# Kernel optimization log

Hardware: AMD Instinct MI355X
Metric: run time of the kernel (lower is better)

Reference implementation:

```python
import jax, jax.numpy as jnp
import numpy as np

B, MAXN = 4096, 10
NVT, MAXPOS = 26, 9          # max_pos + 1
HS, NZ = 301, 56
EMB, FEAT = 16, 8
VS = HS + MAXPOS             # hidden || pos one-hot fed to gate/mapper
XDIM = NVT + MAXPOS          # GRU input dim
DF = 3 * MAXPOS              # r/c/gm per position
GS = HS + FEAT


def _gru(x, h, W_ih, W_hh, b_ih, b_hh):
    # torch.nn.GRUCell semantics (gate order r, z, n)
    gi = x @ W_ih.T + b_ih
    gh = h @ W_hh.T + b_hh
    ir, iz, inn = jnp.split(gi, 3, axis=-1)
    hr, hz, hn = jnp.split(gh, 3, axis=-1)
    rg = jax.nn.sigmoid(ir + hr)
    zg = jax.nn.sigmoid(iz + hz)
    ng = jnp.tanh(inn + rg * hn)
    return (1.0 - zg) * ng + zg * h


def setup_inputs() -> dict:
    key = jax.random.key(0)
    ks = jax.random.split(key, 32)
    def gl(k, shape, fan_in):
        return (jax.random.normal(k, shape, jnp.float32) / np.sqrt(fan_in)).astype(jnp.float32)
    inp = {
        'node_type': jax.random.randint(ks[0], (B, MAXN), 0, NVT),
        'pos':       jax.random.randint(ks[1], (B, MAXN), 0, MAXPOS),
        'adj':       jax.random.randint(ks[2], (B, MAXN, MAXN), 0, 2).astype(jnp.int32),
        'vcount':    jax.random.randint(ks[3], (B,), 0, MAXN),
        'r':  jax.random.uniform(ks[4], (B, MAXN), jnp.float32),
        'c':  jax.random.uniform(ks[5], (B, MAXN), jnp.float32),
        'gm': jax.random.uniform(ks[6], (B, MAXN), jnp.float32),
        # grue_forward (GRUCell)
        'W_ih': gl(ks[7], (3 * HS, XDIM), XDIM),
        'W_hh': gl(ks[8], (3 * HS, HS), HS),
        'b_ih': jnp.zeros((3 * HS,), jnp.float32),
        'b_hh': jnp.zeros((3 * HS,), jnp.float32),
        # gate_forward (Linear + sigmoid) and mapper_forward (Linear, no bias)
        'Wg': gl(ks[9], (HS, VS), VS),
        'bg': jnp.zeros((HS,), jnp.float32),
        'Wm': gl(ks[10], (HS, VS), VS),
        # df_enc: Linear(27,16) ReLU Linear(16,8)
        'W1': gl(ks[11], (EMB, DF), DF),
        'b1': jnp.zeros((EMB,), jnp.float32),
        'W2': gl(ks[12], (FEAT, EMB), EMB),
        'b2': jnp.zeros((FEAT,), jnp.float32),
        # fc1 / fc2 heads
        'Wmu': gl(ks[13], (NZ, GS), GS),
        'bmu': jnp.zeros((NZ,), jnp.float32),
        'Wlv': gl(ks[14], (NZ, GS), GS),
        'blv': jnp.zeros((NZ,), jnp.float32),
    }
    return inp


def reference(node_type, pos, adj, vcount, r, c, gm,
              W_ih, W_hh, b_ih, b_hh, Wg, bg, Wm,
              W1, b1, W2, b2, Wmu, bmu, Wlv, blv):
    n = jnp.clip(vcount, 1, MAXN).astype(jnp.int32)          # graphs have >=1 vertex
    node_ids = jnp.arange(MAXN)
    valid = node_ids[None, :] < n[:, None]                   # [B, MAXN] vertex exists
    tri = node_ids[:, None] < node_ids[None, :]              # u < v (topological DAG)
    A = (adj.astype(jnp.float32) * tri
         * valid[:, :, None] * valid[:, None, :])            # [B, u, v] pred mask

    t_oh = jax.nn.one_hot(node_type, NVT, dtype=jnp.float32)
    p_oh = jax.nn.one_hot(pos, MAXPOS, dtype=jnp.float32)
    X = jnp.concatenate([t_oh, p_oh], axis=-1)               # [B, MAXN, XDIM]

    H = jnp.zeros((B, MAXN, HS), jnp.float32)
    for v in range(MAXN):
        if v == 0:
            Hin = jnp.zeros((B, HS), jnp.float32)            # H0 in encode()
        else:
            # gated predecessor aggregation: sum_u gate(h_u||pos_u)*mapper(h_u||pos_u)
            Hcat = jnp.concatenate([H[:, :v], p_oh[:, :v]], axis=-1)   # [B, v, VS]
            gated = (jax.nn.sigmoid(jnp.einsum('bud,hd->buh', Hcat, Wg) + bg)
                     * jnp.einsum('bud,hd->buh', Hcat, Wm))            # [B, v, HS]
            Hin = jnp.einsum('bu,buh->bh', A[:, :v, v], gated)
        Hv = _gru(X[:, v], Hin, W_ih, W_hh, b_ih, b_hh)
        H = H.at[:, v].set(jnp.where(valid[:, v][:, None], Hv, H[:, v]))

    # graph state: H_forward of last existing vertex
    Hg = H[jnp.arange(B), n - 1]                             # [B, HS]

    # df feature: per-position (r, c, gm), later vertices overwrite earlier ones
    df = jnp.zeros((B, DF), jnp.float32)
    bi = jnp.arange(B)
    for v in range(MAXN):
        m = valid[:, v][:, None]
        for k, val in enumerate((r[:, v], c[:, v], gm[:, v])):
            upd = df.at[bi, pos[:, v] * 3 + k].set(val)
            df = jnp.where(m, upd, df)

    Hd = jax.nn.relu(df @ W1.T + b1) @ W2.T + b2             # df_enc
    Hfull = jnp.concatenate([Hg, Hd], axis=-1)               # [B, GS]
    mu = Hfull @ Wmu.T + bmu
    logvar = Hfull @ Wlv.T + blv
    return mu, logvar
```

## Files before the change

kernel.cpp:

```cpp
#include <hip/hip_runtime.h>
#include <hip/hip_bf16.h>


#define HS 301
#define NVT 26
#define MAXPOS 9
#define MAXN 10
#define BSZ 4096
#define VS 310
#define GS 309
#define NZ 56

#define KT1 11
#define KT2 10
#define NJT 19
#define NB1 (NJT*KT1*3*512)
#define NB2 (NJT*KT2*2*512)

typedef _Float16 f16x8 __attribute__((ext_vector_type(8)));
typedef float f32x4 __attribute__((ext_vector_type(4)));

constexpr int NTH  = 1024;
constexpr int BT   = 16;
constexpr int NBLK = 256;

__device__ __forceinline__ int fragOff(int g, int k) {
  return ((k >> 5) << 10) + ((((k & 31) >> 3) << 4) + g) * 16 + ((k & 7) << 1);
}
__device__ __forceinline__ float sigm(float x) { return 1.0f / (1.0f + __expf(-x)); }
__device__ __forceinline__ float tanh_fast(float x) {
  float e = __expf(2.0f * x);
  return 1.0f - 2.0f / (e + 1.0f);
}
#define BC(x) __builtin_bit_cast(f16x8, (x))

__global__ void ckt_sort(const int* __restrict__ vcount, int* __restrict__ order) {
  __shared__ int cnt[12], off[12];
  int tid = threadIdx.x;
  if (tid < 12) cnt[tid] = 0;
  __syncthreads();
  for (int g = tid; g < BSZ; g += 1024) {
    int n = vcount[g]; n = n < 1 ? 1 : (n > MAXN ? MAXN : n);
    atomicAdd(&cnt[n], 1);
  }
  __syncthreads();
  if (tid == 0) {
    int s = 0;
    for (int i = 1; i <= MAXN; ++i) { off[i] = s; s += cnt[i]; }
  }
  __syncthreads();
  for (int g = tid; g < BSZ; g += 1024) {
    int n = vcount[g]; n = n < 1 ? 1 : (n > MAXN ? MAXN : n);
    int p = atomicAdd(&off[n], 1);
    order[p] = g;
  }
}

__global__ void ckt_prep(const float* __restrict__ Wih, const float* __restrict__ Whh,
                         const float* __restrict__ b_ih, const float* __restrict__ b_hh,
                         const float* __restrict__ Wg,  const float* __restrict__ bg,
                         const float* __restrict__ Wm,
                         const float* __restrict__ Wmu, const float* __restrict__ Wlv,
                         unsigned short* __restrict__ B1, unsigned short* __restrict__ B2,
                         float* __restrict__ WnX, float* __restrict__ bn,
                         float* __restrict__ WmuT, float* __restrict__ WlvT)
{
  int i0 = blockIdx.x * blockDim.x + threadIdx.x;
  int str = gridDim.x * blockDim.x;
  for (int i = i0; i < NB1; i += str) {
    int ii = i & 7, lane = (i >> 3) & 63;
    int r = i >> 9;
    int g3 = r % 3; r /= 3;
    int kt = r % KT1; int jt = r / KT1;
    int j = jt * 16 + (lane & 15);
    int k = kt * 32 + ((lane >> 4) << 3) + ii;
    float val = 0.f;
    if (j < HS) {
      int row = g3 * HS + j;
      if (k < HS) val = Whh[row * HS + k];
      else if (k == 336) val = (g3 < 2) ? (b_ih[row] + b_hh[row]) : b_hh[row];
      else if (g3 < 2) {
        if (k < 327)      val = Wih[row * 35 + (k - 301)];
        else if (k < 336) val = Wih[row * 35 + 26 + (k - 327)];
      }
    }
    B1[i] = __builtin_bit_cast(unsigned short, (_Float16)val);
  }
  for (int i = i0; i < NB2; i += str) {
    int ii = i & 7, lane = (i >> 3) & 63;
    int r = i >> 9;
    int gm = r % 2; r /= 2;
    int kt = r % KT2; int jt = r / KT2;
    int j = jt * 16 + (lane & 15);
    int k = kt * 32 + ((lane >> 4) << 3) + ii;
    float val = 0.f;
    if (j < HS) {
      const float* W = gm ? Wm : Wg;
      if (k < HS)       val = W[j * VS + k];
      else if (k < 310) val = W[j * VS + HS + (k - 301)];
      else if (k == 310) val = gm ? 0.f : bg[j];
    }
    B2[i] = __builtin_bit_cast(unsigned short, (_Float16)val);
  }
  for (int i = i0; i < 35 * 320; i += str) {
    int x = i / 320, j = i % 320;
    WnX[i] = (j < HS) ? Wih[(2 * HS + j) * 35 + x] : 0.f;
  }
  for (int i = i0; i < 320; i += str) bn[i] = (i < HS) ? b_ih[2 * HS + i] : 0.f;
  for (int i = i0; i < GS * NZ; i += str) {
    int k = i / NZ, o = i % NZ;
    WmuT[i] = Wmu[o * GS + k];
    WlvT[i] = Wlv[o * GS + k];
  }
}

__global__ __launch_bounds__(NTH) void ckt_main(
    const int* __restrict__ node_type, const int* __restrict__ pos,
    const int* __restrict__ adj, const int* __restrict__ vcount,
    const float* __restrict__ rin, const float* __restrict__ cin,
    const float* __restrict__ gmin,
    const float* __restrict__ W1, const float* __restrict__ b1,
    const float* __restrict__ W2, const float* __restrict__ b2,
    const float* __restrict__ bmu, const float* __restrict__ blv,
    const uint4* __restrict__ B1, const uint4* __restrict__ B2,
    const float* __restrict__ WnX, const float* __restrict__ bnG,
    const float* __restrict__ WmuT, const float* __restrict__ WlvT,
    const int* __restrict__ order,
    float* __restrict__ out)
{
  __shared__ __align__(16) _Float16 sGhist[9 * 16 * 304];
  __shared__ __align__(16) char sAf1[KT1 * 1024];
  __shared__ __align__(16) char sAf2[KT2 * 1024];
  __shared__ __align__(16) _Float16 sHg[16 * 304];
  __shared__ float sBn[320];
  __shared__ int s_gi[16];
  __shared__ int s_t[160], s_p[160], s_n[16];
  __shared__ unsigned s_am[160];
  __shared__ int s_nmax;
  __shared__ float s_df[16][28];
  __shared__ float s_hd[16][16];
  __shared__ float s_hd2[16][8];

  const int tid  = threadIdx.x;
  const int b0   = blockIdx.x * BT;
  const int w    = tid >> 6;
  const int lane = tid & 63;

  if (tid < 16) s_gi[tid] = order[b0 + tid];
  __syncthreads();
  if (tid < 16) {
    int n = vcount[s_gi[tid]];
    s_n[tid] = n < 1 ? 1 : (n > MAXN ? MAXN : n);
    sHg[tid * 304 + 301] = (_Float16)0.f;
    sHg[tid * 304 + 302] = (_Float16)0.f;
    sHg[tid * 304 + 303] = (_Float16)0.f;
  }
  if (tid < 160) {
    int g = tid / 10, vv = tid % 10;
    s_t[tid] = node_type[s_gi[g] * MAXN + vv];
    s_p[tid] = pos[s_gi[g] * MAXN + vv];
  }
  if (tid < 320) sBn[tid] = bnG[tid];
  __syncthreads();
  if (tid < 160) {
    int g = tid / 10, vv = tid % 10;
    unsigned m = 0;
    if (vv < s_n[g]) {
      for (int u = 0; u < vv; ++u)
        if (adj[s_gi[g] * 100 + u * 10 + vv]) m |= (1u << u);
    }
    s_am[tid] = m;
  }
  if (tid == 0) {
    int mx = 1;
    for (int g = 0; g < 16; ++g) mx = max(mx, s_n[g]);
    s_nmax = mx;
  }
  __syncthreads();
  const int nmax = s_nmax;

  const int lq4 = (lane >> 4) << 2;
  const int jc  = lane & 15;

  for (int v = 0; v < nmax; ++v) {
    if (tid < KT1 * 64) {
      int c = tid;
      int kt = c >> 6, ln = c & 63, g = ln & 15;
      int k0 = (kt << 5) + ((ln >> 4) << 3);
      unsigned am = s_am[g * 10 + v];
      f16x8 pk;
      if (k0 + 8 <= HS) {
        float a0 = 0.f, a1 = 0.f, a2 = 0.f, a3 = 0.f;
        float a4 = 0.f, a5 = 0.f, a6 = 0.f, a7 = 0.f;
        for (int u = 0; u < v; ++u) {
          float mf = (float)((am >> u) & 1u);
          f16x8 hh = *(const f16x8*)(sGhist + (u * 16 + g) * 304 + k0);
          a0 += mf * (float)hh[0]; a1 += mf * (float)hh[1];
          a2 += mf * (float)hh[2]; a3 += mf * (float)hh[3];
          a4 += mf * (float)hh[4]; a5 += mf * (float)hh[5];
          a6 += mf * (float)hh[6]; a7 += mf * (float)hh[7];
        }
        pk[0] = (_Float16)a0; pk[1] = (_Float16)a1;
        pk[2] = (_Float16)a2; pk[3] = (_Float16)a3;
        pk[4] = (_Float16)a4; pk[5] = (_Float16)a5;
        pk[6] = (_Float16)a6; pk[7] = (_Float16)a7;
      } else {
        int t = s_t[g * 10 + v], p = s_p[g * 10 + v];
        #pragma unroll
        for (int e = 0; e < 8; ++e) {
          int k = k0 + e;
          float x = 0.f;
          if (k < HS) {
            for (int u = 0; u < v; ++u) {
              float mf = (float)((am >> u) & 1u);
              x += mf * (float)sGhist[(u * 16 + g) * 304 + k];
            }
          } else if (k < 327) x = (k - 301 == t) ? 1.f : 0.f;
          else if (k < 336)   x = (k - 327 == p) ? 1.f : 0.f;
          else if (k == 336)  x = 1.f;
          pk[e] = (_Float16)x;
        }
      }
      *(f16x8*)(sAf1 + c * 16) = pk;
    } else if (tid - KT1 * 64 < 16 * 19) {
      int i = tid - KT1 * 64;
      int g = i / 19, kk = 301 + i % 19;
      float val = (kk < 310) ? ((kk - 301 == s_p[g * 10 + v]) ? 1.f : 0.f)
                             : ((kk == 310) ? 1.f : 0.f);
      *(_Float16*)(sAf2 + fragOff(g, kk)) = (_Float16)val;
    }
    __syncthreads();

#define LB1(P0, P1, P2, KT) \
      P0 = BC(Bp[((KT) * 3 + 0) * 64]); \
      P1 = BC(Bp[((KT) * 3 + 1) * 64]); \
      P2 = BC(Bp[((KT) * 3 + 2) * 64]);
#define ST1(P0, P1, P2, KT, KTN) { \
      f16x8 av = *(const f16x8*)(sAf1 + (KT) * 1024 + lane * 16); \
      f16x8 c0 = P0, c1 = P1, c2 = P2; \
      LB1(P0, P1, P2, KTN) \
      a0 = __builtin_amdgcn_mfma_f32_16x16x32_f16(av, c0, a0, 0, 0, 0); \
      a1 = __builtin_amdgcn_mfma_f32_16x16x32_f16(av, c1, a1, 0, 0, 0); \
      a2 = __builtin_amdgcn_mfma_f32_16x16x32_f16(av, c2, a2, 0, 0, 0); }
#define ST1E(P0, P1, P2, KT) { \
      f16x8 av = *(const f16x8*)(sAf1 + (KT) * 1024 + lane * 16); \
      a0 = __builtin_amdgcn_mfma_f32_16x16x32_f16(av, P0, a0, 0, 0, 0); \
      a1 = __builtin_amdgcn_mfma_f32_16x16x32_f16(av, P1, a1, 0, 0, 0); \
      a2 = __builtin_amdgcn_mfma_f32_16x16x32_f16(av, P2, a2, 0, 0, 0); }
    for (int jj = w; jj < NJT; jj += 16) {
      const uint4* Bp = B1 + (size_t)jj * (KT1 * 3 * 64) + lane;
      f16x8 p00, p01, p02, p10, p11, p12, p20, p21, p22, p30, p31, p32;
      LB1(p00, p01, p02, 0) LB1(p10, p11, p12, 1)
      LB1(p20, p21, p22, 2) LB1(p30, p31, p32, 3)
      f32x4 a0 = {0.f, 0.f, 0.f, 0.f}, a1 = a0, a2 = a0;
      ST1(p00, p01, p02, 0, 4) ST1(p10, p11, p12, 1, 5)
      ST1(p20, p21, p22, 2, 6) ST1(p30, p31, p32, 3, 7)
      ST1(p00, p01, p02, 4, 8) ST1(p10, p11, p12, 5, 9)
      ST1(p20, p21, p22, 6, 10)
      ST1E(p30, p31, p32, 7) ST1E(p00, p01, p02, 8)
      ST1E(p10, p11, p12, 9) ST1E(p20, p21, p22, 10)
      int j = jj * 16 + jc;
      bool jv = j < HS;
      #pragma unroll
      for (int q = 0; q < 4; ++q) {
        int g = lq4 + q;
        float inn = 0.f;
        if (jv) {
          int t = s_t[g * 10 + v], p = s_p[g * 10 + v];
          inn = sBn[j] + WnX[t * 320 + j] + WnX[(26 + p) * 320 + j];
        }
        float rg = sigm(a0[q]);
        float zg = sigm(a1[q]);
        float ng = tanh_fast(inn + rg * a2[q]);
        float hinv = jv ? (float)*(const _Float16*)(sAf1 + fragOff(g, j)) : 0.f;
        float hv = (1.f - zg) * ng + zg * hinv;
        float hval = (v < s_n[g]) ? hv : 0.f;
        if (jv) {
          *(_Float16*)(sAf2 + fragOff(g, j)) = (_Float16)hval;
          if (v == s_n[g] - 1) sHg[g * 304 + j] = (_Float16)hv;
        }
      }
    }
#undef ST1
#undef ST1E
#undef LB1
    __syncthreads();

    if (v < nmax - 1) {
#define LB2(P0, P1, KT) \
        P0 = BC(Bp[((KT) * 2 + 0) * 64]); \
        P1 = BC(Bp[((KT) * 2 + 1) * 64]);
#define ST2(P0, P1, KT, KTN) { \
        f16x8 av = *(const f16x8*)(sAf2 + (KT) * 1024 + lane * 16); \
        f16x8 d0 = P0, d1 = P1; \
        LB2(P0, P1, KTN) \
        c0 = __builtin_amdgcn_mfma_f32_16x16x32_f16(av, d0, c0, 0, 0, 0); \
        c1 = __builtin_amdgcn_mfma_f32_16x16x32_f16(av, d1, c1, 0, 0, 0); }
#define ST2E(P0, P1, KT) { \
        f16x8 av = *(const f16x8*)(sAf2 + (KT) * 1024 + lane * 16); \
        c0 = __builtin_amdgcn_mfma_f32_16x16x32_f16(av, P0, c0, 0, 0, 0); \
        c1 = __builtin_amdgcn_mfma_f32_16x16x32_f16(av, P1, c1, 0, 0, 0); }
      for (int jj = w; jj < NJT; jj += 16) {
        const uint4* Bp = B2 + (size_t)jj * (KT2 * 2 * 64) + lane;
        f16x8 q00, q01, q10, q11, q20, q21, q30, q31;
        LB2(q00, q01, 0) LB2(q10, q11, 1) LB2(q20, q21, 2) LB2(q30, q31, 3)
        f32x4 c0 = {0.f, 0.f, 0.f, 0.f}, c1 = c0;
        ST2(q00, q01, 0, 4) ST2(q10, q11, 1, 5) ST2(q20, q21, 2, 6)
        ST2(q30, q31, 3, 7) ST2(q00, q01, 4, 8) ST2(q10, q11, 5, 9)
        ST2E(q20, q21, 6) ST2E(q30, q31, 7) ST2E(q00, q01, 8) ST2E(q10, q11, 9)
        int j = jj * 16 + jc;
        if (j < HS) {
          #pragma unroll
          for (int q = 0; q < 4; ++q) {
            int g = lq4 + q;
            float gg = sigm(c0[q]);
            sGhist[(v * 16 + g) * 304 + j] = (_Float16)(gg * c1[q]);
          }
        }
      }
#undef ST2
#undef ST2E
#undef LB2
    }
    __syncthreads();
  }

  if (tid < 16) {
    int g = tid;
    #pragma unroll
    for (int i2 = 0; i2 < 27; ++i2) s_df[g][i2] = 0.f;
    int n = s_n[g];
    int gi = s_gi[g];
    for (int vv = 0; vv < n; ++vv) {
      int p = s_p[g * 10 + vv];
      int base = gi * MAXN + vv;
      s_df[g][3 * p]     = rin[base];
      s_df[g][3 * p + 1] = cin[base];
      s_df[g][3 * p + 2] = gmin[base];
    }
  }
  __syncthreads();

  if (tid < 256) {
    int bb = tid >> 4, o = tid & 15;
    float a = b1[o];
    #pragma unroll
    for (int k = 0; k < 27; ++k) a = fmaf(W1[o * 27 + k], s_df[bb][k], a);
    s_hd[bb][o] = fmaxf(a, 0.f);
  }
  __syncthreads();
  if (tid < 128) {
    int bb = tid >> 3, o = tid & 7;
    float a = b2[o];
    #pragma unroll
    for (int k = 0; k < 16; ++k) a = fmaf(W2[o * 16 + k], s_hd[bb][k], a);
    s_hd2[bb][o] = a;
  }
  __syncthreads();

  if (tid < 2 * NZ) {
    bool ismu = tid < NZ;
    int oo = ismu ? tid : tid - NZ;
    const float* WT = ismu ? WmuT : WlvT;
    float acc[16];
    #pragma unroll
    for (int g = 0; g < 16; ++g) acc[g] = 0.f;
    for (int k0 = 0; k0 < 304; k0 += 8) {
      float wv[8];
      #pragma unroll
      for (int e = 0; e < 8; ++e) {
        int k = k0 + e;
        wv[e] = (k < HS) ? WT[k * NZ + oo] : 0.f;
      }
      #pragma unroll
      for (int g = 0; g < 16; ++g) {
        f16x8 hh = *(const f16x8*)(sHg + g * 304 + k0);
        #pragma unroll
        for (int e = 0; e < 8; ++e) acc[g] += wv[e] * (float)hh[e];
      }
    }
    #pragma unroll
    for (int g = 0; g < 16; ++g) {
      float a = acc[g];
      #pragma unroll
      for (int kk = 0; kk < 8; ++kk) a += WT[(HS + kk) * NZ + oo] * s_hd2[g][kk];
      a += ismu ? bmu[oo] : blv[oo];
      out[(ismu ? 0 : BSZ * NZ) + s_gi[g] * NZ + oo] = a;
    }
  }
}

extern "C" void kernel_launch(void* const* d_in, const int* in_sizes, int n_in,
                              void* d_out, int out_size, void* d_ws, size_t ws_size,
                              hipStream_t stream) {
  const int*   node_type = (const int*)d_in[0];
  const int*   pos       = (const int*)d_in[1];
  const int*   adj       = (const int*)d_in[2];
  const int*   vcount    = (const int*)d_in[3];
  const float* rin       = (const float*)d_in[4];
  const float* cin       = (const float*)d_in[5];
  const float* gmin      = (const float*)d_in[6];
  const float* Wih       = (const float*)d_in[7];
  const float* Whh       = (const float*)d_in[8];
  const float* b_ih      = (const float*)d_in[9];
  const float* b_hh      = (const float*)d_in[10];
  const float* Wg        = (const float*)d_in[11];
  const float* bg        = (const float*)d_in[12];
  const float* Wm        = (const float*)d_in[13];
  const float* W1        = (const float*)d_in[14];
  const float* b1        = (const float*)d_in[15];
  const float* W2        = (const float*)d_in[16];
  const float* b2        = (const float*)d_in[17];
  const float* Wmu       = (const float*)d_in[18];
  const float* bmu       = (const float*)d_in[19];
  const float* Wlv       = (const float*)d_in[20];
  const float* blv       = (const float*)d_in[21];

  char* wsb = (char*)d_ws;
  unsigned short* B1 = (unsigned short*)wsb;
  unsigned short* B2 = (unsigned short*)(wsb + 642048);
  float* WnX  = (float*)(wsb + 1031168);
  float* bn   = (float*)(wsb + 1075968);
  float* WmuT = (float*)(wsb + 1077248);
  float* WlvT = (float*)(wsb + 1146464);
  int*   order = (int*)(wsb + 1215680);

  ckt_prep<<<512, 256, 0, stream>>>(Wih, Whh, b_ih, b_hh, Wg, bg, Wm, Wmu, Wlv,
                                    B1, B2, WnX, bn, WmuT, WlvT);
  ckt_sort<<<1, 1024, 0, stream>>>(vcount, order);

  ckt_main<<<NBLK, NTH, 0, stream>>>(node_type, pos, adj, vcount, rin, cin, gmin,
      W1, b1, W2, b2, bmu, blv,
      (const uint4*)B1, (const uint4*)B2, WnX, bn, WmuT, WlvT, order, (float*)d_out);
}
```

Measured before the change: 162.2 us.

## Prefetch MFMA weight fragments across barriers and use LDS-only barrier waits

Issues the global loads for the first weight k-tiles of each wave's GRU and gate GEMMs before the preceding barrier, so their latency overlaps the A-fragment build and the GRU epilogue. The strided jj loops are split into an always-run first tile and a conditional second tile for waves 0-2. __syncthreads is replaced by an lgkmcnt-only wait plus s_barrier, so in-flight global loads are not drained at barriers. A waves_per_eu(4) attribute is added. Together these raise register pressure and lean on the hand-written waitcnt being correct.

```diff
diff --git a/kernel.cpp b/kernel.cpp
--- a/kernel.cpp
+++ b/kernel.cpp
@@ -33,6 +33,8 @@
   return 1.0f - 2.0f / (e + 1.0f);
 }
 #define BC(x) __builtin_bit_cast(f16x8, (x))
+#define BAR() { asm volatile("s_waitcnt lgkmcnt(0)" ::: "memory"); \
+                __builtin_amdgcn_s_barrier(); }
 
 __global__ void ckt_sort(const int* __restrict__ vcount, int* __restrict__ order) {
   __shared__ int cnt[12], off[12];
@@ -114,7 +116,9 @@
   }
 }
 
-__global__ __launch_bounds__(NTH) void ckt_main(
+__global__ __launch_bounds__(NTH)
+__attribute__((amdgpu_waves_per_eu(4)))
+void ckt_main(
     const int* __restrict__ node_type, const int* __restrict__ pos,
     const int* __restrict__ adj, const int* __restrict__ vcount,
     const float* __restrict__ rin, const float* __restrict__ cin,
@@ -181,8 +185,14 @@
 
   const int lq4 = (lane >> 4) << 2;
   const int jc  = lane & 15;
+  const uint4* BpW = B1 + (size_t)w * (KT1 * 3 * 64) + lane;
+  const uint4* BqW = B2 + (size_t)w * (KT2 * 2 * 64) + lane;
 
   for (int v = 0; v < nmax; ++v) {
+    f16x8 f00 = BC(BpW[0]),   f01 = BC(BpW[64]),  f02 = BC(BpW[128]);
+    f16x8 f10 = BC(BpW[192]), f11 = BC(BpW[256]), f12 = BC(BpW[320]);
+    f16x8 g00, g01, g10, g11;
+
     if (tid < KT1 * 64) {
       int c = tid;
       int kt = c >> 6, ln = c & 63, g = ln & 15;
@@ -229,7 +239,7 @@
                              : ((kk == 310) ? 1.f : 0.f);
       *(_Float16*)(sAf2 + fragOff(g, kk)) = (_Float16)val;
     }
-    __syncthreads();
+    BAR();
 
 #define LB1(P0, P1, P2, KT) \
       P0 = BC(Bp[((KT) * 3 + 0) * 64]); \
@@ -247,8 +257,44 @@
       a0 = __builtin_amdgcn_mfma_f32_16x16x32_f16(av, P0, a0, 0, 0, 0); \
       a1 = __builtin_amdgcn_mfma_f32_16x16x32_f16(av, P1, a1, 0, 0, 0); \
       a2 = __builtin_amdgcn_mfma_f32_16x16x32_f16(av, P2, a2, 0, 0, 0); }
-    for (int jj = w; jj < NJT; jj += 16) {
-      const uint4* Bp = B1 + (size_t)jj * (KT1 * 3 * 64) + lane;
+#define GRU_EPI(JT) { \
+      int j = (JT) * 16 + jc; \
+      bool jv = j < HS; \
+      _Pragma("unroll") \
+      for (int q = 0; q < 4; ++q) { \
+        int g = lq4 + q; \
+        float inn = 0.f; \
+        if (jv) { \
+          int t = s_t[g * 10 + v], p = s_p[g * 10 + v]; \
+          inn = sBn[j] + WnX[t * 320 + j] + WnX[(26 + p) * 320 + j]; \
+        } \
+        float rg = sigm(a0[q]); \
+        float zg = sigm(a1[q]); \
+        float ng = tanh_fast(inn + rg * a2[q]); \
+        float hinv = jv ? (float)*(const _Float16*)(sAf1 + fragOff(g, j)) : 0.f; \
+        float hv = (1.f - zg) * ng + zg * hinv; \
+        float hval = (v < s_n[g]) ? hv : 0.f; \
+        if (jv) { \
+          *(_Float16*)(sAf2 + fragOff(g, j)) = (_Float16)hval; \
+          if (v == s_n[g] - 1) sHg[g * 304 + j] = (_Float16)hv; \
+        } \
+      } }
+    {
+      const uint4* Bp = BpW;
+      f16x8 p20, p21, p22, p30, p31, p32;
+      LB1(p20, p21, p22, 2) LB1(p30, p31, p32, 3)
+      f32x4 a0 = {0.f, 0.f, 0.f, 0.f}, a1 = a0, a2 = a0;
+      ST1(f00, f01, f02, 0, 4) ST1(f10, f11, f12, 1, 5)
+      ST1(p20, p21, p22, 2, 6) ST1(p30, p31, p32, 3, 7)
+      ST1(f00, f01, f02, 4, 8) ST1(f10, f11, f12, 5, 9)
+      ST1(p20, p21, p22, 6, 10)
+      ST1E(p30, p31, p32, 7) ST1E(f00, f01, f02, 8)
+      ST1E(f10, f11, f12, 9) ST1E(p20, p21, p22, 10)
+      GRU_EPI(w)
+    }
+    if (w < 3) {
+      const int jt2 = w + 16;
+      const uint4* Bp = B1 + (size_t)jt2 * (KT1 * 3 * 64) + lane;
       f16x8 p00, p01, p02, p10, p11, p12, p20, p21, p22, p30, p31, p32;
       LB1(p00, p01, p02, 0) LB1(p10, p11, p12, 1)
       LB1(p20, p21, p22, 2) LB1(p30, p31, p32, 3)
@@ -259,32 +305,14 @@
       ST1(p20, p21, p22, 6, 10)
       ST1E(p30, p31, p32, 7) ST1E(p00, p01, p02, 8)
       ST1E(p10, p11, p12, 9) ST1E(p20, p21, p22, 10)
-      int j = jj * 16 + jc;
-      bool jv = j < HS;
-      #pragma unroll
-      for (int q = 0; q < 4; ++q) {
-        int g = lq4 + q;
-        float inn = 0.f;
-        if (jv) {
-          int t = s_t[g * 10 + v], p = s_p[g * 10 + v];
-          inn = sBn[j] + WnX[t * 320 + j] + WnX[(26 + p) * 320 + j];
-        }
-        float rg = sigm(a0[q]);
-        float zg = sigm(a1[q]);
-        float ng = tanh_fast(inn + rg * a2[q]);
-        float hinv = jv ? (float)*(const _Float16*)(sAf1 + fragOff(g, j)) : 0.f;
-        float hv = (1.f - zg) * ng + zg * hinv;
-        float hval = (v < s_n[g]) ? hv : 0.f;
-        if (jv) {
-          *(_Float16*)(sAf2 + fragOff(g, j)) = (_Float16)hval;
-          if (v == s_n[g] - 1) sHg[g * 304 + j] = (_Float16)hv;
-        }
-      }
+      GRU_EPI(jt2)
     }
 #undef ST1
 #undef ST1E
 #undef LB1
-    __syncthreads();
+    g00 = BC(BqW[0]);   g01 = BC(BqW[64]);
+    g10 = BC(BqW[128]); g11 = BC(BqW[192]);
+    BAR();
 
     if (v < nmax - 1) {
 #define LB2(P0, P1, KT) \
@@ -300,29 +328,42 @@
         f16x8 av = *(const f16x8*)(sAf2 + (KT) * 1024 + lane * 16); \
         c0 = __builtin_amdgcn_mfma_f32_16x16x32_f16(av, P0, c0, 0, 0, 0); \
         c1 = __builtin_amdgcn_mfma_f32_16x16x32_f16(av, P1, c1, 0, 0, 0); }
-      for (int jj = w; jj < NJT; jj += 16) {
-        const uint4* Bp = B2 + (size_t)jj * (KT2 * 2 * 64) + lane;
+#define GATE_EPI(JT) { \
+        int j = (JT) * 16 + jc; \
+        if (j < HS) { \
+          _Pragma("unroll") \
+          for (int q = 0; q < 4; ++q) { \
+            int g = lq4 + q; \
+            float gg = sigm(c0[q]); \
+            sGhist[(v * 16 + g) * 304 + j] = (_Float16)(gg * c1[q]); \
+          } \
+        } }
+      {
+        const uint4* Bp = BqW;
+        f16x8 q20, q21, q30, q31;
+        LB2(q20, q21, 2) LB2(q30, q31, 3)
+        f32x4 c0 = {0.f, 0.f, 0.f, 0.f}, c1 = c0;
+        ST2(g00, g01, 0, 4) ST2(g10, g11, 1, 5) ST2(q20, q21, 2, 6)
+        ST2(q30, q31, 3, 7) ST2(g00, g01, 4, 8) ST2(g10, g11, 5, 9)
+        ST2E(q20, q21, 6) ST2E(q30, q31, 7) ST2E(g00, g01, 8) ST2E(g10, g11, 9)
+        GATE_EPI(w)
+      }
+      if (w < 3) {
+        const int jt2 = w + 16;
+        const uint4* Bp = B2 + (size_t)jt2 * (KT2 * 2 * 64) + lane;
         f16x8 q00, q01, q10, q11, q20, q21, q30, q31;
         LB2(q00, q01, 0) LB2(q10, q11, 1) LB2(q20, q21, 2) LB2(q30, q31, 3)
         f32x4 c0 = {0.f, 0.f, 0.f, 0.f}, c1 = c0;
         ST2(q00, q01, 0, 4) ST2(q10, q11, 1, 5) ST2(q20, q21, 2, 6)
         ST2(q30, q31, 3, 7) ST2(q00, q01, 4, 8) ST2(q10, q11, 5, 9)
         ST2E(q20, q21, 6) ST2E(q30, q31, 7) ST2E(q00, q01, 8) ST2E(q10, q11, 9)
-        int j = jj * 16 + jc;
-        if (j < HS) {
-          #pragma unroll
-          for (int q = 0; q < 4; ++q) {
-            int g = lq4 + q;
-            float gg = sigm(c0[q]);
-            sGhist[(v * 16 + g) * 304 + j] = (_Float16)(gg * c1[q]);
-          }
-        }
+        GATE_EPI(jt2)
       }
 #undef ST2
 #undef ST2E
 #undef LB2
     }
-    __syncthreads();
+    BAR();
   }
 
   if (tid < 16) {
```

Measured after the change: 452.7 us. +179.1%, slower.

## Shrink block to four waves with deeper B prefetch and lighter barriers

Applied to the files above, without the earlier changes.

Cuts the main kernel from 1024 to 256 threads per block and requests a single block per CU via launch bounds. Each wave now loops over up to five 16-column j-tiles instead of at most two. The weight-fragment prefetch for both MFMA GEMMs becomes a six- or five-stage register pipeline. __syncthreads is replaced by an explicit lgkmcnt wait plus s_barrier. The aim is cheaper barriers and more registers for deeper prefetch, at the cost of fewer waves to hide latency and a longer serial chain per wave in each recurrence step.

```diff
diff --git a/kernel.cpp b/kernel.cpp
--- a/kernel.cpp
+++ b/kernel.cpp
@@ -20,7 +20,7 @@
 typedef _Float16 f16x8 __attribute__((ext_vector_type(8)));
 typedef float f32x4 __attribute__((ext_vector_type(4)));
 
-constexpr int NTH  = 1024;
+constexpr int NTH  = 256;
 constexpr int BT   = 16;
 constexpr int NBLK = 256;
 
@@ -33,6 +33,8 @@
   return 1.0f - 2.0f / (e + 1.0f);
 }
 #define BC(x) __builtin_bit_cast(f16x8, (x))
+#define BAR() { asm volatile("s_waitcnt lgkmcnt(0)" ::: "memory"); \
+                __builtin_amdgcn_s_barrier(); }
 
 __global__ void ckt_sort(const int* __restrict__ vcount, int* __restrict__ order) {
   __shared__ int cnt[12], off[12];
@@ -114,7 +116,7 @@
   }
 }
 
-__global__ __launch_bounds__(NTH) void ckt_main(
+__global__ __launch_bounds__(NTH, 1) void ckt_main(
     const int* __restrict__ node_type, const int* __restrict__ pos,
     const int* __restrict__ adj, const int* __restrict__ vcount,
     const float* __restrict__ rin, const float* __restrict__ cin,
@@ -160,7 +162,7 @@
     s_t[tid] = node_type[s_gi[g] * MAXN + vv];
     s_p[tid] = pos[s_gi[g] * MAXN + vv];
   }
-  if (tid < 320) sBn[tid] = bnG[tid];
+  for (int k = tid; k < 320; k += NTH) sBn[k] = bnG[k];
   __syncthreads();
   if (tid < 160) {
     int g = tid / 10, vv = tid % 10;
@@ -183,8 +185,7 @@
   const int jc  = lane & 15;
 
   for (int v = 0; v < nmax; ++v) {
-    if (tid < KT1 * 64) {
-      int c = tid;
+    for (int c = tid; c < KT1 * 64; c += NTH) {
       int kt = c >> 6, ln = c & 63, g = ln & 15;
       int k0 = (kt << 5) + ((ln >> 4) << 3);
       unsigned am = s_am[g * 10 + v];
@@ -222,43 +223,41 @@
         }
       }
       *(f16x8*)(sAf1 + c * 16) = pk;
-    } else if (tid - KT1 * 64 < 16 * 19) {
-      int i = tid - KT1 * 64;
+    }
+    for (int i = tid; i < 16 * 19; i += NTH) {
       int g = i / 19, kk = 301 + i % 19;
       float val = (kk < 310) ? ((kk - 301 == s_p[g * 10 + v]) ? 1.f : 0.f)
                              : ((kk == 310) ? 1.f : 0.f);
       *(_Float16*)(sAf2 + fragOff(g, kk)) = (_Float16)val;
     }
-    __syncthreads();
-
-#define LB1(P0, P1, P2, KT) \
-      P0 = BC(Bp[((KT) * 3 + 0) * 64]); \
-      P1 = BC(Bp[((KT) * 3 + 1) * 64]); \
-      P2 = BC(Bp[((KT) * 3 + 2) * 64]);
-#define ST1(P0, P1, P2, KT, KTN) { \
+    BAR();
+
+#define LD1(S0, S1, S2, KT) \
+      S0 = BC(Bp[((KT) * 3 + 0) * 64]); \
+      S1 = BC(Bp[((KT) * 3 + 1) * 64]); \
+      S2 = BC(Bp[((KT) * 3 + 2) * 64]);
+#define MF1(S0, S1, S2, KT) { \
       f16x8 av = *(const f16x8*)(sAf1 + (KT) * 1024 + lane * 16); \
-      f16x8 c0 = P0, c1 = P1, c2 = P2; \
-      LB1(P0, P1, P2, KTN) \
-      a0 = __builtin_amdgcn_mfma_f32_16x16x32_f16(av, c0, a0, 0, 0, 0); \
-      a1 = __builtin_amdgcn_mfma_f32_16x16x32_f16(av, c1, a1, 0, 0, 0); \
-      a2 = __builtin_amdgcn_mfma_f32_16x16x32_f16(av, c2, a2, 0, 0, 0); }
-#define ST1E(P0, P1, P2, KT) { \
-      f16x8 av = *(const f16x8*)(sAf1 + (KT) * 1024 + lane * 16); \
-      a0 = __builtin_amdgcn_mfma_f32_16x16x32_f16(av, P0, a0, 0, 0, 0); \
-      a1 = __builtin_amdgcn_mfma_f32_16x16x32_f16(av, P1, a1, 0, 0, 0); \
-      a2 = __builtin_amdgcn_mfma_f32_16x16x32_f16(av, P2, a2, 0, 0, 0); }
-    for (int jj = w; jj < NJT; jj += 16) {
+      a0 = __builtin_amdgcn_mfma_f32_16x16x32_f16(av, S0, a0, 0, 0, 0); \
+      a1 = __builtin_amdgcn_mfma_f32_16x16x32_f16(av, S1, a1, 0, 0, 0); \
+      a2 = __builtin_amdgcn_mfma_f32_16x16x32_f16(av, S2, a2, 0, 0, 0); }
+    for (int r = 0; r < 5; ++r) {
+      int jj = w + 4 * r;
+      if (jj >= NJT) break;
       const uint4* Bp = B1 + (size_t)jj * (KT1 * 3 * 64) + lane;
-      f16x8 p00, p01, p02, p10, p11, p12, p20, p21, p22, p30, p31, p32;
-      LB1(p00, p01, p02, 0) LB1(p10, p11, p12, 1)
-      LB1(p20, p21, p22, 2) LB1(p30, p31, p32, 3)
+      f16x8 s00,s01,s02, s10,s11,s12, s20,s21,s22,
+            s30,s31,s32, s40,s41,s42, s50,s51,s52;
+      LD1(s00,s01,s02, 0) LD1(s10,s11,s12, 1) LD1(s20,s21,s22, 2)
+      LD1(s30,s31,s32, 3) LD1(s40,s41,s42, 4) LD1(s50,s51,s52, 5)
       f32x4 a0 = {0.f, 0.f, 0.f, 0.f}, a1 = a0, a2 = a0;
-      ST1(p00, p01, p02, 0, 4) ST1(p10, p11, p12, 1, 5)
-      ST1(p20, p21, p22, 2, 6) ST1(p30, p31, p32, 3, 7)
-      ST1(p00, p01, p02, 4, 8) ST1(p10, p11, p12, 5, 9)
-      ST1(p20, p21, p22, 6, 10)
-      ST1E(p30, p31, p32, 7) ST1E(p00, p01, p02, 8)
-      ST1E(p10, p11, p12, 9) ST1E(p20, p21, p22, 10)
+      MF1(s00,s01,s02, 0)  LD1(s00,s01,s02, 6)
+      MF1(s10,s11,s12, 1)  LD1(s10,s11,s12, 7)
+      MF1(s20,s21,s22, 2)  LD1(s20,s21,s22, 8)
+      MF1(s30,s31,s32, 3)  LD1(s30,s31,s32, 9)
+      MF1(s40,s41,s42, 4)  LD1(s40,s41,s42, 10)
+      MF1(s50,s51,s52, 5)
+      MF1(s00,s01,s02, 6)  MF1(s10,s11,s12, 7)  MF1(s20,s21,s22, 8)
+      MF1(s30,s31,s32, 9)  MF1(s40,s41,s42, 10)
       int j = jj * 16 + jc;
       bool jv = j < HS;
       #pragma unroll
@@ -281,33 +280,33 @@
         }
       }
     }
-#undef ST1
-#undef ST1E
-#undef LB1
-    __syncthreads();
+#undef LD1
+#undef MF1
+    BAR();
 
     if (v < nmax - 1) {
-#define LB2(P0, P1, KT) \
-        P0 = BC(Bp[((KT) * 2 + 0) * 64]); \
-        P1 = BC(Bp[((KT) * 2 + 1) * 64]);
-#define ST2(P0, P1, KT, KTN) { \
+#define LD2(S0, S1, KT) \
+        S0 = BC(Bp[((KT) * 2 + 0) * 64]); \
+        S1 = BC(Bp[((KT) * 2 + 1) * 64]);
+#define MF2(S0, S1, KT) { \
         f16x8 av = *(const f16x8*)(sAf2 + (KT) * 1024 + lane * 16); \
-        f16x8 d0 = P0, d1 = P1; \
-        LB2(P0, P1, KTN) \
-        c0 = __builtin_amdgcn_mfma_f32_16x16x32_f16(av, d0, c0, 0, 0, 0); \
-        c1 = __builtin_amdgcn_mfma_f32_16x16x32_f16(av, d1, c1, 0, 0, 0); }
-#define ST2E(P0, P1, KT) { \
-        f16x8 av = *(const f16x8*)(sAf2 + (KT) * 1024 + lane * 16); \
-        c0 = __builtin_amdgcn_mfma_f32_16x16x32_f16(av, P0, c0, 0, 0, 0); \
-        c1 = __builtin_amdgcn_mfma_f32_16x16x32_f16(av, P1, c1, 0, 0, 0); }
-      for (int jj = w; jj < NJT; jj += 16) {
+        c0 = __builtin_amdgcn_mfma_f32_16x16x32_f16(av, S0, c0, 0, 0, 0); \
+        c1 = __builtin_amdgcn_mfma_f32_16x16x32_f16(av, S1, c1, 0, 0, 0); }
+      for (int r = 0; r < 5; ++r) {
+        int jj = w + 4 * r;
+        if (jj >= NJT) break;
         const uint4* Bp = B2 + (size_t)jj * (KT2 * 2 * 64) + lane;
-        f16x8 q00, q01, q10, q11, q20, q21, q30, q31;
-        LB2(q00, q01, 0) LB2(q10, q11, 1) LB2(q20, q21, 2) LB2(q30, q31, 3)
+        f16x8 q00,q01, q10,q11, q20,q21, q30,q31, q40,q41;
+        LD2(q00,q01, 0) LD2(q10,q11, 1) LD2(q20,q21, 2)
+        LD2(q30,q31, 3) LD2(q40,q41, 4)
         f32x4 c0 = {0.f, 0.f, 0.f, 0.f}, c1 = c0;
-        ST2(q00, q01, 0, 4) ST2(q10, q11, 1, 5) ST2(q20, q21, 2, 6)
-        ST2(q30, q31, 3, 7) ST2(q00, q01, 4, 8) ST2(q10, q11, 5, 9)
-        ST2E(q20, q21, 6) ST2E(q30, q31, 7) ST2E(q00, q01, 8) ST2E(q10, q11, 9)
+        MF2(q00,q01, 0)  LD2(q00,q01, 5)
+        MF2(q10,q11, 1)  LD2(q10,q11, 6)
+        MF2(q20,q21, 2)  LD2(q20,q21, 7)
+        MF2(q30,q31, 3)  LD2(q30,q31, 8)
+        MF2(q40,q41, 4)  LD2(q40,q41, 9)
+        MF2(q00,q01, 5)  MF2(q10,q11, 6)  MF2(q20,q21, 7)
+        MF2(q30,q31, 8)  MF2(q40,q41, 9)
         int j = jj * 16 + jc;
         if (j < HS) {
           #pragma unroll
@@ -318,11 +317,10 @@
           }
         }
       }
-#undef ST2
-#undef ST2E
-#undef LB2
-    }
-    __syncthreads();
+#undef LD2
+#undef MF2
+    }
+    BAR();
   }
 
   if (tid < 16) {
@@ -341,7 +339,7 @@
   }
   __syncthreads();
 
-  if (tid < 256) {
+  {
     int bb = tid >> 4, o = tid & 15;
     float a = b1[o];
     #pragma unroll
```

After: 211.9 us. 1.31x slower.
